# Performance work log

Hardware: AMD Instinct MI355X
Metric: run time of the kernel (lower is better)

Reference implementation:

```python
import jax, jax.numpy as jnp
import numpy as np

H = 1024        # hidden_size
I = 512         # moe_intermediate_size
E = 16          # n_routed_experts
K = 2           # num_experts_per_tok
N_SHARED = 2    # n_shared_experts
IS = I * N_SHARED  # shared expert intermediate
B, S = 2, 2048


def setup_inputs() -> dict:
    key = jax.random.key(0)
    ks = jax.random.split(key, 9)
    sc = 0.02
    return {
        "hidden_states": jax.random.normal(ks[0], (B, S, H), jnp.float32),
        "router_w":     jax.random.normal(ks[1], (E, H), jnp.float32) * sc,
        "expert_gate":  jax.random.normal(ks[2], (E, H, I), jnp.float32) * sc,
        "expert_up":    jax.random.normal(ks[3], (E, H, I), jnp.float32) * sc,
        "expert_down":  jax.random.normal(ks[4], (E, I, H), jnp.float32) * sc,
        "shared_gate":  jax.random.normal(ks[5], (H, IS), jnp.float32) * sc,
        "shared_up":    jax.random.normal(ks[6], (H, IS), jnp.float32) * sc,
        "shared_down":  jax.random.normal(ks[7], (IS, H), jnp.float32) * sc,
    }


def reference(hidden_states, router_w, expert_gate, expert_up, expert_down,
              shared_gate, shared_up, shared_down):
    orig_shape = hidden_states.shape
    x = hidden_states.reshape(-1, H)            # [T, H]
    T = x.shape[0]

    # --- MoEGate: softmax router scores, top-k, normalized weights ---
    scores = jax.nn.softmax(x @ router_w.T, axis=-1)        # [T, E]
    topk_w, topk_idx = jax.lax.top_k(scores, K)             # [T, K]
    topk_w = topk_w / jnp.sum(topk_w, axis=-1, keepdims=True)  # norm_topk_prob

    # Sparse combine weights as dense [T, E] gate matrix (scatter of top-k).
    gates = jnp.zeros((T, E), x.dtype).at[jnp.arange(T)[:, None], topk_idx].add(topk_w)

    # --- Routed experts: gated SiLU MLP per expert, weighted combine ---
    g = jnp.einsum('th,ehi->tei', x, expert_gate)           # [T, E, I]
    u = jnp.einsum('th,ehi->tei', x, expert_up)             # [T, E, I]
    a = jax.nn.silu(g) * u                                  # [T, E, I]
    y = jnp.einsum('tei,eih,te->th', a, expert_down, gates) # [T, H]

    # --- Shared experts ---
    s = (jax.nn.silu(x @ shared_gate) * (x @ shared_up)) @ shared_down  # [T, H]

    return (y + s).reshape(orig_shape)
```

## Files before the change

### kernel.cpp

```cpp
#include <hip/hip_runtime.h>
#include <hip/hip_bf16.h>
#include <math.h>

#define H_DIM 1024
#define I_DIM 512
#define E_NUM 16
#define T_TOK 4096
#define IS_DIM 1024
#define CSTR 32

#define P_RT   1024
#define P_WU   (P_RT + 2048)
#define P_SG   (P_WU + 2048)
#define P_SU   (P_SG + 256)
#define P_WD   (P_SU + 256)
#define P_SD   (P_WD + 2048)
#define P_END  (P_SD + 256)

#define G_GEMM 1152
#define D_GRID 896

typedef unsigned short u16;
typedef __attribute__((ext_vector_type(8))) short short8;
typedef __attribute__((ext_vector_type(4))) float floatx4;

__device__ __forceinline__ float bf2f(u16 u) {
    union { unsigned int u; float f; } c; c.u = ((unsigned int)u) << 16; return c.f;
}
__device__ __forceinline__ u16 f2bf(float f) {
    union { __hip_bfloat16 b; u16 u; } c;
    c.b = __float2bfloat16(f);
    return c.u;
}
__device__ __forceinline__ void gld16(const u16* g, u16* l) {
    __builtin_amdgcn_global_load_lds(
        (const __attribute__((address_space(1))) unsigned int*)g,
        (__attribute__((address_space(3))) unsigned int*)l, 16, 0, 0);
}

__device__ __forceinline__ void tr64(const float* src, u16* dst, int R, int C,
                                     int local, u16* tile)
{
    int tpm = (R >> 6) * (C >> 6);
    int mat = local / tpm;
    int tl_ = local - mat * tpm;
    int tcn = C >> 6;
    int tr = tl_ / tcn, tc = tl_ - tr * tcn;
    src += (size_t)mat * R * C;
    dst += (size_t)mat * R * C;
    int t = threadIdx.x;
    int r0 = t >> 2, g0 = t & 3;
    const float* sp = src + (size_t)(tr * 64 + r0) * C + tc * 64 + (g0 << 4);
    u16 cv[16];
    #pragma unroll
    for (int j = 0; j < 16; j += 4) {
        float4 v = *(const float4*)(sp + j);
        cv[j + 0] = f2bf(v.x);
        cv[j + 1] = f2bf(v.y);
        cv[j + 2] = f2bf(v.z);
        cv[j + 3] = f2bf(v.w);
    }
    u16* tp = tile + r0 * 72 + ((g0 ^ (r0 >> 4)) << 4);
    *(short8*)(tp)     = *(const short8*)(cv);
    *(short8*)(tp + 8) = *(const short8*)(cv + 8);
    __syncthreads();
    int cW = t >> 2, rW = (t & 3) << 4;
    int rb = (((cW >> 4) ^ (t & 3)) << 4) + (cW & 15);
    u16 tmp[16];
    #pragma unroll
    for (int j = 0; j < 16; ++j) tmp[j] = tile[(rW + j) * 72 + rb];
    u16* dp = dst + (size_t)(tc * 64 + cW) * R + tr * 64 + rW;
    *(uint4*)(dp)     = *(const uint4*)(tmp);
    *(uint4*)(dp + 8) = *(const uint4*)(tmp + 8);
}

__device__ __forceinline__ int derive_routed(int gi, const int* cnt,
                                             int& e, int& mt, int& sub, int& abase)
{
    int off = 0, b = 0;
    #pragma unroll
    for (int ee = 0; ee < E_NUM; ++ee) {
        int mts = (cnt[ee * CSTR] + 127) >> 7;
        int span = mts << 3;
        if (gi < off + span) {
            int local = gi - off;
            e = ee; mt = local >> 3; sub = local & 7; abase = b;
            return 1;
        }
        off += span; b += mts << 7;
    }
    return 0;
}

__global__ __launch_bounds__(256, 6)
void k_prep(const float* x, const float* rw,
            const float* wg, const float* wu, const float* sg, const float* su,
            const float* wd, const float* sd,
            u16* wgt, u16* wut, u16* sgt, u16* sut, u16* wdt, u16* sdt,
            u16* xb, float* topkw, int* elist, int* cnt)
{
    __shared__ u16 tile[64 * 72];
    int bi = blockIdx.x;
    if (bi >= P_RT) {
        if (bi < P_WU)      tr64(wg, wgt, 1024, 512,  bi - P_RT, tile);
        else if (bi < P_SG) tr64(wu, wut, 1024, 512,  bi - P_WU, tile);
        else if (bi < P_SU) tr64(sg, sgt, 1024, 1024, bi - P_SG, tile);
        else if (bi < P_WD) tr64(su, sut, 1024, 1024, bi - P_SU, tile);
        else if (bi < P_SD) tr64(wd, wdt, 512, 1024,  bi - P_WD, tile);
        else                tr64(sd, sdt, 1024, 1024, bi - P_SD, tile);
        return;
    }
    int lane = threadIdx.x & 63;
    int wv = threadIdx.x >> 6;
    int t = bi * 4 + wv;
    const float* xr = x + (size_t)t * H_DIM;
    float xv[16];
    #pragma unroll
    for (int j = 0; j < 16; ++j) xv[j] = xr[j * 64 + lane];
    u16* xrow = xb + (size_t)t * H_DIM;
    #pragma unroll
    for (int j = 0; j < 16; ++j) xrow[j * 64 + lane] = f2bf(xv[j]);
    float sc[E_NUM];
    #pragma unroll
    for (int e = 0; e < E_NUM; ++e) sc[e] = 0.f;
    #pragma unroll
    for (int e = 0; e < E_NUM; ++e) {
        const float* rr = rw + e * H_DIM;
        #pragma unroll
        for (int j = 0; j < 16; ++j) sc[e] += xv[j] * rr[j * 64 + lane];
    }
    #pragma unroll
    for (int off = 32; off > 0; off >>= 1) {
        float tmp[E_NUM];
        #pragma unroll
        for (int e = 0; e < E_NUM; ++e) tmp[e] = __shfl_xor(sc[e], off, 64);
        #pragma unroll
        for (int e = 0; e < E_NUM; ++e) sc[e] += tmp[e];
    }
    if (lane == 0) {
        float b1 = -1e30f, b2 = -1e30f; int i1 = 0, i2 = 0;
        #pragma unroll
        for (int e = 0; e < E_NUM; ++e) {
            if (sc[e] > b1) { b2 = b1; i2 = i1; b1 = sc[e]; i1 = e; }
            else if (sc[e] > b2) { b2 = sc[e]; i2 = e; }
        }
        float w1 = 1.f / (1.f + __expf(b2 - b1));
        float w2 = 1.f - w1;
        topkw[t * 2]     = w1;
        topkw[t * 2 + 1] = w2;
        int p1 = atomicAdd(&cnt[i1 * CSTR], 1); elist[i1 * T_TOK + p1] = (t << 1);
        int p2 = atomicAdd(&cnt[i2 * CSTR], 1); elist[i2 * T_TOK + p2] = (t << 1) | 1;
    }
}

__global__ __launch_bounds__(256, 3)
void k_gateup(const u16* xb, const u16* wgt, const u16* wut,
              const u16* sgt, const u16* sut,
              const int* elist, const int* cnt,
              u16* act, u16* sact)
{
    __shared__ u16 smem[128 * 64 + 64 * 64 + 64 * 64];
    int bi = blockIdx.x;
    int kind, e = 0, mt, cb, abase = 0;
    if (bi < 512) { kind = 1; mt = bi >> 4; cb = bi & 15; }
    else {
        kind = 0;
        if (!derive_routed(bi - 512, cnt, e, mt, cb, abase)) return;
    }

    u16* lA = smem;
    u16* lG = smem + 8192;
    u16* lU = smem + 12288;
    int tid = threadIdx.x, lane = tid & 63, w = tid >> 6;
    int srow = lane >> 2, scp = lane & 3;

    const u16* gb = kind ? sgt : (wgt + (size_t)e * I_DIM * H_DIM);
    const u16* ub = kind ? sut : (wut + (size_t)e * I_DIM * H_DIM);
    int c = cnt[e * CSTR];

    const u16 *gA[2], *gG, *gU;
    u16 *dA[2], *dG, *dU;
    #pragma unroll
    for (int jj = 0; jj < 2; ++jj) {
        int call = w * 2 + jj;
        int row = call * 16 + srow;
        int gc = scp ^ ((row >> 1) & 3);
        int tok;
        if (kind) tok = mt * 128 + row;
        else {
            int p = mt * 128 + row;
            int pc = p < c ? p : c - 1;
            tok = elist[e * T_TOK + pc] >> 1;
        }
        gA[jj] = xb + (size_t)tok * H_DIM + gc * 8;
        dA[jj] = lA + call * 512;
    }
    {
        int row = w * 16 + srow;
        int gc = scp ^ ((row >> 1) & 3);
        gG = gb + (size_t)(cb * 64 + row) * H_DIM + gc * 8;
        gU = ub + (size_t)(cb * 64 + row) * H_DIM + gc * 8;
        dG = lG + w * 512;
        dU = lU + w * 512;
    }

    int wr = w >> 1, wc = w & 1;
    int quad = lane >> 4, l15 = lane & 15;
    const u16 *fA[4], *fG[2], *fU[2];
    #pragma unroll
    for (int i = 0; i < 4; ++i) {
        int r = wr * 64 + i * 16 + l15;
        fA[i] = lA + r * 32 + (quad ^ ((r >> 1) & 3)) * 8;
    }
    #pragma unroll
    for (int j = 0; j < 2; ++j) {
        int n = wc * 32 + j * 16 + l15;
        fG[j] = lG + n * 32 + (quad ^ ((n >> 1) & 3)) * 8;
        fU[j] = lU + n * 32 + (quad ^ ((n >> 1) & 3)) * 8;
    }

    floatx4 accg[4][2], accu[4][2];
    #pragma unroll
    for (int i = 0; i < 4; ++i)
        #pragma unroll
        for (int j = 0; j < 2; ++j)
            #pragma unroll
            for (int r = 0; r < 4; ++r) { accg[i][j][r] = 0.f; accu[i][j][r] = 0.f; }

    for (int s = 0; s < H_DIM / 64; ++s) {
        #pragma unroll
        for (int q = 0; q < 2; ++q) {
            gld16(gA[0] + q * 32, dA[0] + q * 4096);
            gld16(gA[1] + q * 32, dA[1] + q * 4096);
            gld16(gG + q * 32, dG + q * 2048);
            gld16(gU + q * 32, dU + q * 2048);
        }
        gA[0] += 64; gA[1] += 64; gG += 64; gU += 64;
        __syncthreads();
        #pragma unroll
        for (int q = 0; q < 2; ++q) {
            short8 a[4], g[2], u[2];
            #pragma unroll
            for (int i = 0; i < 4; ++i) a[i] = *(const short8*)(fA[i] + q * 4096);
            #pragma unroll
            for (int j = 0; j < 2; ++j) {
                g[j] = *(const short8*)(fG[j] + q * 2048);
                u[j] = *(const short8*)(fU[j] + q * 2048);
            }
            #pragma unroll
            for (int i = 0; i < 4; ++i)
                #pragma unroll
                for (int j = 0; j < 2; ++j) {
                    accg[i][j] = __builtin_amdgcn_mfma_f32_16x16x32_bf16(a[i], g[j], accg[i][j], 0, 0, 0);
                    accu[i][j] = __builtin_amdgcn_mfma_f32_16x16x32_bf16(a[i], u[j], accu[i][j], 0, 0, 0);
                }
        }
        __syncthreads();
    }

    u16* obase = kind ? (sact + (size_t)(mt * 128) * IS_DIM)
                      : (act + (size_t)(abase + mt * 128) * I_DIM);
    int old = kind ? IS_DIM : I_DIM;
    #pragma unroll
    for (int i = 0; i < 4; ++i)
        #pragma unroll
        for (int j = 0; j < 2; ++j)
            #pragma unroll
            for (int r = 0; r < 4; ++r) {
                int row = wr * 64 + i * 16 + quad * 4 + r;
                int col = cb * 64 + wc * 32 + j * 16 + l15;
                float gg = accg[i][j][r], uu = accu[i][j][r];
                float aa = gg / (1.f + __expf(-gg)) * uu;
                obase[(size_t)row * old + col] = f2bf(aa);
            }
}

__global__ __launch_bounds__(256, 3)
void k_down(const u16* act, const u16* sact, const u16* wdt, const u16* sdt,
            const int* elist, const int* cnt, const float* topkw,
            u16* y0, u16* y1, float* out)
{
    int bi = blockIdx.x;
    int kind, e = 0, mt, nb, abase = 0;
    if (bi < 256) { kind = 1; mt = bi >> 3; nb = bi & 7; }
    else {
        kind = 0;
        if (!derive_routed(bi - 256, cnt, e, mt, nb, abase)) return;
    }

    __shared__ u16 smem[128 * 64 * 2];
    u16* lA = smem;
    u16* lB = smem + 8192;
    int tid = threadIdx.x, lane = tid & 63, w = tid >> 6;
    int srow = lane >> 2, scp = lane & 3;

    int K = kind ? IS_DIM : I_DIM;
    const u16* ab = kind ? (sact + (size_t)(mt * 128) * IS_DIM)
                         : (act + (size_t)(abase + mt * 128) * I_DIM);
    const u16* bb = kind ? (sdt + (size_t)(nb * 128) * IS_DIM)
                         : (wdt + ((size_t)e * H_DIM + nb * 128) * I_DIM);
    int c = cnt[e * CSTR];

    const u16 *gA[2], *gB[2];
    u16 *dA[2], *dB[2];
    #pragma unroll
    for (int jj = 0; jj < 2; ++jj) {
        int call = w * 2 + jj;
        int row = call * 16 + srow;
        int gc = scp ^ ((row >> 1) & 3);
        gA[jj] = ab + (size_t)row * K + gc * 8;
        dA[jj] = lA + call * 512;
        gB[jj] = bb + (size_t)row * K + gc * 8;
        dB[jj] = lB + call * 512;
    }

    int wr = w >> 1, wc = w & 1;
    int quad = lane >> 4, l15 = lane & 15;
    const u16 *fA[4], *fB[4];
    #pragma unroll
    for (int i = 0; i < 4; ++i) {
        int r = wr * 64 + i * 16 + l15;
        fA[i] = lA + r * 32 + (quad ^ ((r >> 1) & 3)) * 8;
    }
    #pragma unroll
    for (int j = 0; j < 4; ++j) {
        int n = wc * 64 + j * 16 + l15;
        fB[j] = lB + n * 32 + (quad ^ ((n >> 1) & 3)) * 8;
    }

    floatx4 acc[4][4];
    #pragma unroll
    for (int i = 0; i < 4; ++i)
        #pragma unroll
        for (int j = 0; j < 4; ++j)
            #pragma unroll
            for (int r = 0; r < 4; ++r) acc[i][j][r] = 0.f;

    int steps = K >> 6;
    for (int s = 0; s < steps; ++s) {
        #pragma unroll
        for (int q = 0; q < 2; ++q) {
            gld16(gA[0] + q * 32, dA[0] + q * 4096);
            gld16(gA[1] + q * 32, dA[1] + q * 4096);
            gld16(gB[0] + q * 32, dB[0] + q * 4096);
            gld16(gB[1] + q * 32, dB[1] + q * 4096);
        }
        gA[0] += 64; gA[1] += 64; gB[0] += 64; gB[1] += 64;
        __syncthreads();
        #pragma unroll
        for (int q = 0; q < 2; ++q) {
            short8 a[4], b[4];
            #pragma unroll
            for (int i = 0; i < 4; ++i) a[i] = *(const short8*)(fA[i] + q * 4096);
            #pragma unroll
            for (int j = 0; j < 4; ++j) b[j] = *(const short8*)(fB[j] + q * 4096);
            #pragma unroll
            for (int i = 0; i < 4; ++i)
                #pragma unroll
                for (int j = 0; j < 4; ++j)
                    acc[i][j] = __builtin_amdgcn_mfma_f32_16x16x32_bf16(a[i], b[j], acc[i][j], 0, 0, 0);
        }
        __syncthreads();
    }

    if (kind) {
        #pragma unroll
        for (int i = 0; i < 4; ++i)
            #pragma unroll
            for (int j = 0; j < 4; ++j)
                #pragma unroll
                for (int r = 0; r < 4; ++r) {
                    int row = mt * 128 + wr * 64 + i * 16 + quad * 4 + r;
                    int col = nb * 128 + wc * 64 + j * 16 + l15;
                    out[(size_t)row * H_DIM + col] = acc[i][j][r];
                }
    } else {
        #pragma unroll
        for (int i = 0; i < 4; ++i)
            #pragma unroll
            for (int r = 0; r < 4; ++r) {
                int row = wr * 64 + i * 16 + quad * 4 + r;
                int p = mt * 128 + row;
                if (p < c) {
                    int ent = elist[e * T_TOK + p];
                    int t = ent >> 1, sl = ent & 1;
                    float wt = topkw[t * 2 + sl];
                    u16* yb = sl ? y1 : y0;
                    #pragma unroll
                    for (int j = 0; j < 4; ++j) {
                        int col = nb * 128 + wc * 64 + j * 16 + l15;
                        yb[(size_t)t * H_DIM + col] = f2bf(wt * acc[i][j][r]);
                    }
                }
            }
    }
}

__global__ __launch_bounds__(256)
void k_final(float* out, const u16* y0, const u16* y1)
{
    int i = blockIdx.x * 256 + threadIdx.x;
    float4 o = ((const float4*)out)[i];
    uint2 a = ((const uint2*)y0)[i];
    uint2 b = ((const uint2*)y1)[i];
    const u16* pa = (const u16*)&a;
    const u16* pb = (const u16*)&b;
    o.x += bf2f(pa[0]) + bf2f(pb[0]);
    o.y += bf2f(pa[1]) + bf2f(pb[1]);
    o.z += bf2f(pa[2]) + bf2f(pb[2]);
    o.w += bf2f(pa[3]) + bf2f(pb[3]);
    ((float4*)out)[i] = o;
}

extern "C" void kernel_launch(void* const* d_in, const int* in_sizes, int n_in,
                              void* d_out, int out_size, void* d_ws, size_t ws_size,
                              hipStream_t stream)
{
    const float* x  = (const float*)d_in[0];
    const float* rw = (const float*)d_in[1];
    const float* wg = (const float*)d_in[2];
    const float* wu = (const float*)d_in[3];
    const float* wd = (const float*)d_in[4];
    const float* sg = (const float*)d_in[5];
    const float* su = (const float*)d_in[6];
    const float* sd = (const float*)d_in[7];
    float* out = (float*)d_out;

    char* ws = (char*)d_ws;
    const size_t MB = 1024ull * 1024ull;
    u16* wgt  = (u16*)(ws);
    u16* wut  = (u16*)(ws + 16 * MB);
    u16* wdt  = (u16*)(ws + 32 * MB);
    u16* sgt  = (u16*)(ws + 48 * MB);
    u16* sut  = (u16*)(ws + 50 * MB);
    u16* sdt  = (u16*)(ws + 52 * MB);
    u16* xb   = (u16*)(ws + 54 * MB);
    u16* act  = (u16*)(ws + 62 * MB);
    u16* sact = (u16*)(ws + 72 * MB);
    u16* y0   = (u16*)(ws + 80 * MB);
    u16* y1   = (u16*)(ws + 88 * MB);
    float* topkw  = (float*)(ws + 96 * MB);
    int* elist    = (int*)(ws + 96 * MB + 64 * 1024);
    int* cnt      = (int*)(ws + 97 * MB);

    hipMemsetAsync(cnt, 0, E_NUM * CSTR * sizeof(int), stream);
    k_prep<<<P_END, 256, 0, stream>>>(x, rw, wg, wu, sg, su, wd, sd,
                                      wgt, wut, sgt, sut, wdt, sdt,
                                      xb, topkw, elist, cnt);
    k_gateup<<<G_GEMM, 256, 0, stream>>>(xb, wgt, wut, sgt, sut,
                                         elist, cnt, act, sact);
    k_down<<<D_GRID, 256, 0, stream>>>(act, sact, wdt, sdt,
                                       elist, cnt, topkw, y0, y1, out);
    k_final<<<T_TOK * H_DIM / 4 / 256, 256, 0, stream>>>(out, y0, y1);
}
```

Measured before the change: 266.0 us.

## Fuse final combine into down kernel via atomic completion counter

Removes the separate k_final kernel. Routed down blocks are reordered to run first and each bumps a global done counter when finished. Shared-expert blocks then spin until every routed block has signalled, and write out = acc + y0 + y1 directly, which saves one fp32 read-modify-write pass over the output and a kernel launch. This relies on the routed blocks being scheduled ahead of the spinning blocks (otherwise it could deadlock), and the spin-wait can leave CUs idle.

```diff
diff --git a/kernel.cpp b/kernel.cpp
--- a/kernel.cpp
+++ b/kernel.cpp
@@ -18,7 +18,8 @@
 #define P_END  (P_SD + 256)
 
 #define G_GEMM 1152
-#define D_GRID 896
+#define DR_N   640
+#define D_GRID (DR_N + 256)
 
 typedef unsigned short u16;
 typedef __attribute__((ext_vector_type(8))) short short8;
@@ -157,10 +158,11 @@
 void k_gateup(const u16* xb, const u16* wgt, const u16* wut,
               const u16* sgt, const u16* sut,
               const int* elist, const int* cnt,
-              u16* act, u16* sact)
+              u16* act, u16* sact, int* done)
 {
     __shared__ u16 smem[128 * 64 + 64 * 64 + 64 * 64];
     int bi = blockIdx.x;
+    if (bi == 0 && threadIdx.x == 0) *done = 0;
     int kind, e = 0, mt, cb, abase = 0;
     if (bi < 512) { kind = 1; mt = bi >> 4; cb = bi & 15; }
     else {
@@ -278,20 +280,28 @@
 __global__ __launch_bounds__(256, 3)
 void k_down(const u16* act, const u16* sact, const u16* wdt, const u16* sdt,
             const int* elist, const int* cnt, const float* topkw,
-            u16* y0, u16* y1, float* out)
+            u16* y0, u16* y1, float* out, int* done)
 {
     int bi = blockIdx.x;
+    int tid = threadIdx.x, lane = tid & 63, w = tid >> 6;
     int kind, e = 0, mt, nb, abase = 0;
-    if (bi < 256) { kind = 1; mt = bi >> 3; nb = bi & 7; }
-    else {
+    if (bi < DR_N) {
         kind = 0;
-        if (!derive_routed(bi - 256, cnt, e, mt, nb, abase)) return;
+        if (!derive_routed(bi, cnt, e, mt, nb, abase)) {
+            if (tid == 0)
+                __hip_atomic_fetch_add(done, 1, __ATOMIC_RELEASE,
+                                       __HIP_MEMORY_SCOPE_AGENT);
+            return;
+        }
+    } else {
+        kind = 1;
+        int v = bi - DR_N;
+        mt = v >> 3; nb = v & 7;
     }
 
     __shared__ u16 smem[128 * 64 * 2];
     u16* lA = smem;
     u16* lB = smem + 8192;
-    int tid = threadIdx.x, lane = tid & 63, w = tid >> 6;
     int srow = lane >> 2, scp = lane & 3;
 
     int K = kind ? IS_DIM : I_DIM;
@@ -363,18 +373,7 @@
         __syncthreads();
     }
 
-    if (kind) {
-        #pragma unroll
-        for (int i = 0; i < 4; ++i)
-            #pragma unroll
-            for (int j = 0; j < 4; ++j)
-                #pragma unroll
-                for (int r = 0; r < 4; ++r) {
-                    int row = mt * 128 + wr * 64 + i * 16 + quad * 4 + r;
-                    int col = nb * 128 + wc * 64 + j * 16 + l15;
-                    out[(size_t)row * H_DIM + col] = acc[i][j][r];
-                }
-    } else {
+    if (!kind) {
         #pragma unroll
         for (int i = 0; i < 4; ++i)
             #pragma unroll
@@ -393,23 +392,32 @@
                     }
                 }
             }
-    }
-}
-
-__global__ __launch_bounds__(256)
-void k_final(float* out, const u16* y0, const u16* y1)
-{
-    int i = blockIdx.x * 256 + threadIdx.x;
-    float4 o = ((const float4*)out)[i];
-    uint2 a = ((const uint2*)y0)[i];
-    uint2 b = ((const uint2*)y1)[i];
-    const u16* pa = (const u16*)&a;
-    const u16* pb = (const u16*)&b;
-    o.x += bf2f(pa[0]) + bf2f(pb[0]);
-    o.y += bf2f(pa[1]) + bf2f(pb[1]);
-    o.z += bf2f(pa[2]) + bf2f(pb[2]);
-    o.w += bf2f(pa[3]) + bf2f(pb[3]);
-    ((float4*)out)[i] = o;
+        __threadfence();
+        __syncthreads();
+        if (tid == 0)
+            __hip_atomic_fetch_add(done, 1, __ATOMIC_RELEASE,
+                                   __HIP_MEMORY_SCOPE_AGENT);
+    } else {
+        if (tid == 0) {
+            while (__hip_atomic_load(done, __ATOMIC_ACQUIRE,
+                                     __HIP_MEMORY_SCOPE_AGENT) < DR_N)
+                __builtin_amdgcn_s_sleep(8);
+        }
+        __syncthreads();
+        __threadfence();
+        #pragma unroll
+        for (int i = 0; i < 4; ++i)
+            #pragma unroll
+            for (int r = 0; r < 4; ++r) {
+                int row = mt * 128 + wr * 64 + i * 16 + quad * 4 + r;
+                #pragma unroll
+                for (int j = 0; j < 4; ++j) {
+                    int col = nb * 128 + wc * 64 + j * 16 + l15;
+                    size_t idx = (size_t)row * H_DIM + col;
+                    out[idx] = acc[i][j][r] + bf2f(y0[idx]) + bf2f(y1[idx]);
+                }
+            }
+    }
 }
 
 extern "C" void kernel_launch(void* const* d_in, const int* in_sizes, int n_in,
@@ -442,14 +450,14 @@
     float* topkw  = (float*)(ws + 96 * MB);
     int* elist    = (int*)(ws + 96 * MB + 64 * 1024);
     int* cnt      = (int*)(ws + 97 * MB);
+    int* done     = (int*)(ws + 97 * MB + 8192);
 
     hipMemsetAsync(cnt, 0, E_NUM * CSTR * sizeof(int), stream);
     k_prep<<<P_END, 256, 0, stream>>>(x, rw, wg, wu, sg, su, wd, sd,
                                       wgt, wut, sgt, sut, wdt, sdt,
                                       xb, topkw, elist, cnt);
     k_gateup<<<G_GEMM, 256, 0, stream>>>(xb, wgt, wut, sgt, sut,
-                                         elist, cnt, act, sact);
+                                         elist, cnt, act, sact, done);
     k_down<<<D_GRID, 256, 0, stream>>>(act, sact, wdt, sdt,
-                                       elist, cnt, topkw, y0, y1, out);
-    k_final<<<T_TOK * H_DIM / 4 / 256, 256, 0, stream>>>(out, y0, y1);
-}
+                                       elist, cnt, topkw, y0, y1, out, done);
+}
```

Measured after the change: 445.1 us. 67.3% more time.

## Fuse MoE stages into one persistent cooperative kernel with grid syncs

Applied to the files above, without the earlier changes.

Replaces the memset and four separate launches (prep, gate/up, down, final) with a single cooperative persistent kernel. Blocks loop over virtual block indices and use grid-wide barriers between stages, which removes launch overhead and inter-kernel gaps. The gate/up and down virtual blocks are also permuted so consecutive physical blocks spread across tiles. In exchange it adds grid.sync costs, fixes occupancy at launch_bounds(256,3) for every stage, and caps the grid at the number of co-resident blocks, so stages with many small blocks run as serial waves.

```diff
diff --git a/kernel.cpp b/kernel.cpp
--- a/kernel.cpp
+++ b/kernel.cpp
@@ -1,6 +1,9 @@
 #include <hip/hip_runtime.h>
 #include <hip/hip_bf16.h>
+#include <hip/hip_cooperative_groups.h>
 #include <math.h>
+
+namespace cg = cooperative_groups;
 
 #define H_DIM 1024
 #define I_DIM 512
@@ -92,15 +95,13 @@
     return 0;
 }
 
-__global__ __launch_bounds__(256, 6)
-void k_prep(const float* x, const float* rw,
+__device__ __forceinline__ void prep_vb(int bi, u16* tile,
+            const float* x, const float* rw,
             const float* wg, const float* wu, const float* sg, const float* su,
             const float* wd, const float* sd,
             u16* wgt, u16* wut, u16* sgt, u16* sut, u16* wdt, u16* sdt,
             u16* xb, float* topkw, int* elist, int* cnt)
 {
-    __shared__ u16 tile[64 * 72];
-    int bi = blockIdx.x;
     if (bi >= P_RT) {
         if (bi < P_WU)      tr64(wg, wgt, 1024, 512,  bi - P_RT, tile);
         else if (bi < P_SG) tr64(wu, wut, 1024, 512,  bi - P_WU, tile);
@@ -153,14 +154,12 @@
     }
 }
 
-__global__ __launch_bounds__(256, 3)
-void k_gateup(const u16* xb, const u16* wgt, const u16* wut,
-              const u16* sgt, const u16* sut,
-              const int* elist, const int* cnt,
-              u16* act, u16* sact)
-{
-    __shared__ u16 smem[128 * 64 + 64 * 64 + 64 * 64];
-    int bi = blockIdx.x;
+__device__ __forceinline__ void gateup_vb(int bi, u16* smem,
+            const u16* xb, const u16* wgt, const u16* wut,
+            const u16* sgt, const u16* sut,
+            const int* elist, const int* cnt,
+            u16* act, u16* sact)
+{
     int kind, e = 0, mt, cb, abase = 0;
     if (bi < 512) { kind = 1; mt = bi >> 4; cb = bi & 15; }
     else {
@@ -275,12 +274,11 @@
             }
 }
 
-__global__ __launch_bounds__(256, 3)
-void k_down(const u16* act, const u16* sact, const u16* wdt, const u16* sdt,
+__device__ __forceinline__ void down_vb(int bi, u16* smem,
+            const u16* act, const u16* sact, const u16* wdt, const u16* sdt,
             const int* elist, const int* cnt, const float* topkw,
             u16* y0, u16* y1, float* out)
 {
-    int bi = blockIdx.x;
     int kind, e = 0, mt, nb, abase = 0;
     if (bi < 256) { kind = 1; mt = bi >> 3; nb = bi & 7; }
     else {
@@ -288,7 +286,6 @@
         if (!derive_routed(bi - 256, cnt, e, mt, nb, abase)) return;
     }
 
-    __shared__ u16 smem[128 * 64 * 2];
     u16* lA = smem;
     u16* lB = smem + 8192;
     int tid = threadIdx.x, lane = tid & 63, w = tid >> 6;
@@ -396,20 +393,54 @@
     }
 }
 
-__global__ __launch_bounds__(256)
-void k_final(float* out, const u16* y0, const u16* y1)
-{
-    int i = blockIdx.x * 256 + threadIdx.x;
-    float4 o = ((const float4*)out)[i];
-    uint2 a = ((const uint2*)y0)[i];
-    uint2 b = ((const uint2*)y1)[i];
-    const u16* pa = (const u16*)&a;
-    const u16* pb = (const u16*)&b;
-    o.x += bf2f(pa[0]) + bf2f(pb[0]);
-    o.y += bf2f(pa[1]) + bf2f(pb[1]);
-    o.z += bf2f(pa[2]) + bf2f(pb[2]);
-    o.w += bf2f(pa[3]) + bf2f(pb[3]);
-    ((float4*)out)[i] = o;
+__global__ __launch_bounds__(256, 3)
+void k_moe(const float* x, const float* rw,
+           const float* wg, const float* wu, const float* wd,
+           const float* sg, const float* su, const float* sd,
+           u16* wgt, u16* wut, u16* sgt, u16* sut, u16* wdt, u16* sdt,
+           u16* xb, float* topkw, int* elist, int* cnt,
+           u16* act, u16* sact, u16* y0, u16* y1, float* out)
+{
+    cg::grid_group grid = cg::this_grid();
+    __shared__ u16 smem[16384];
+    int G = gridDim.x;
+
+    if (blockIdx.x == 0)
+        for (int i = threadIdx.x; i < E_NUM * CSTR; i += 256) cnt[i] = 0;
+    grid.sync();
+
+    for (int vb = blockIdx.x; vb < P_END; vb += G) {
+        prep_vb(vb, smem, x, rw, wg, wu, sg, su, wd, sd,
+                wgt, wut, sgt, sut, wdt, sdt, xb, topkw, elist, cnt);
+        __syncthreads();
+    }
+    grid.sync();
+
+    for (int vb0 = blockIdx.x; vb0 < G_GEMM; vb0 += G) {
+        int vb = (vb0 & 7) * (G_GEMM / 8) + (vb0 >> 3);
+        gateup_vb(vb, smem, xb, wgt, wut, sgt, sut, elist, cnt, act, sact);
+    }
+    grid.sync();
+
+    for (int vb0 = blockIdx.x; vb0 < D_GRID; vb0 += G) {
+        int vb = (vb0 & 7) * (D_GRID / 8) + (vb0 >> 3);
+        down_vb(vb, smem, act, sact, wdt, sdt, elist, cnt, topkw, y0, y1, out);
+    }
+    grid.sync();
+
+    int n4 = T_TOK * H_DIM / 4;
+    for (int i = blockIdx.x * 256 + threadIdx.x; i < n4; i += G * 256) {
+        float4 o = ((const float4*)out)[i];
+        uint2 a = ((const uint2*)y0)[i];
+        uint2 b = ((const uint2*)y1)[i];
+        const u16* pa = (const u16*)&a;
+        const u16* pb = (const u16*)&b;
+        o.x += bf2f(pa[0]) + bf2f(pb[0]);
+        o.y += bf2f(pa[1]) + bf2f(pb[1]);
+        o.z += bf2f(pa[2]) + bf2f(pb[2]);
+        o.w += bf2f(pa[3]) + bf2f(pb[3]);
+        ((float4*)out)[i] = o;
+    }
 }
 
 extern "C" void kernel_launch(void* const* d_in, const int* in_sizes, int n_in,
@@ -439,17 +470,26 @@
     u16* sact = (u16*)(ws + 72 * MB);
     u16* y0   = (u16*)(ws + 80 * MB);
     u16* y1   = (u16*)(ws + 88 * MB);
-    float* topkw  = (float*)(ws + 96 * MB);
-    int* elist    = (int*)(ws + 96 * MB + 64 * 1024);
-    int* cnt      = (int*)(ws + 97 * MB);
-
-    hipMemsetAsync(cnt, 0, E_NUM * CSTR * sizeof(int), stream);
-    k_prep<<<P_END, 256, 0, stream>>>(x, rw, wg, wu, sg, su, wd, sd,
-                                      wgt, wut, sgt, sut, wdt, sdt,
-                                      xb, topkw, elist, cnt);
-    k_gateup<<<G_GEMM, 256, 0, stream>>>(xb, wgt, wut, sgt, sut,
-                                         elist, cnt, act, sact);
-    k_down<<<D_GRID, 256, 0, stream>>>(act, sact, wdt, sdt,
-                                       elist, cnt, topkw, y0, y1, out);
-    k_final<<<T_TOK * H_DIM / 4 / 256, 256, 0, stream>>>(out, y0, y1);
-}
+    float* topkw = (float*)(ws + 96 * MB);
+    int* elist   = (int*)(ws + 96 * MB + 64 * 1024);
+    int* cnt     = (int*)(ws + 97 * MB);
+
+    static int gridBlocks = 0;
+    if (gridBlocks == 0) {
+        int nb = 0;
+        hipOccupancyMaxActiveBlocksPerMultiprocessor(&nb, k_moe, 256, 0);
+        if (nb < 1) nb = 1;
+        if (nb > 8) nb = 8;
+        gridBlocks = nb * 256;
+    }
+
+    void* args[] = { (void*)&x, (void*)&rw, (void*)&wg, (void*)&wu, (void*)&wd,
+                     (void*)&sg, (void*)&su, (void*)&sd,
+                     (void*)&wgt, (void*)&wut, (void*)&sgt, (void*)&sut,
+                     (void*)&wdt, (void*)&sdt,
+                     (void*)&xb, (void*)&topkw, (void*)&elist, (void*)&cnt,
+                     (void*)&act, (void*)&sact, (void*)&y0, (void*)&y1,
+                     (void*)&out };
+    hipLaunchCooperativeKernel((void*)k_moe, dim3(gridBlocks), dim3(256),
+                               args, 0, stream);
+}
```

After: 857.3 us. 222% more time.
